# Kernel optimization log

Measured on AMD Instinct MI355X. Metric: run time of the kernel, lower is better.

The kernel has to match this reference:

```python
import jax, jax.numpy as jnp
import numpy as np

BS, S1, S2, D_IN1, D_IN2, ATTN_DIM, HEADS = 4, 2048, 2048, 512, 512, 512, 8
HEAD_DIM = ATTN_DIM // HEADS
NEG = -1e23


def _layer_norm(x, g, b, eps=1e-5):
    m = jnp.mean(x, axis=-1, keepdims=True)
    v = jnp.mean((x - m) ** 2, axis=-1, keepdims=True)
    return (x - m) / jnp.sqrt(v + eps) * g + b


def setup_inputs() -> dict:
    key = jax.random.key(0)
    ks = jax.random.split(key, 12)
    s = 0.02
    return {
        "modal1": jax.random.normal(ks[0], (BS, S1, D_IN1), dtype=jnp.float32),
        "modal2": jax.random.normal(ks[1], (BS, S2, D_IN2), dtype=jnp.float32),
        "unpadding_mask1": jax.random.randint(ks[2], (BS, S1, 1), 0, 2, dtype=jnp.int32),
        "unpadding_mask2": jax.random.randint(ks[3], (BS, S2), 0, 2, dtype=jnp.int32),
        "Wq": jax.random.normal(ks[4], (D_IN1, ATTN_DIM), dtype=jnp.float32) * s,
        "bq": jnp.zeros((ATTN_DIM,), dtype=jnp.float32),
        "Wkv": jax.random.normal(ks[5], (D_IN2, ATTN_DIM), dtype=jnp.float32) * s,
        "bkv": jnp.zeros((ATTN_DIM,), dtype=jnp.float32),
        "ln1_g": jnp.ones((ATTN_DIM,), dtype=jnp.float32),
        "ln1_b": jnp.zeros((ATTN_DIM,), dtype=jnp.float32),
        "W1": jax.random.normal(ks[6], (ATTN_DIM, ATTN_DIM), dtype=jnp.float32) * s,
        "b1": jnp.zeros((ATTN_DIM,), dtype=jnp.float32),
        "W2": jax.random.normal(ks[7], (ATTN_DIM, ATTN_DIM), dtype=jnp.float32) * s,
        "b2": jnp.zeros((ATTN_DIM,), dtype=jnp.float32),
        "ln2_g": jnp.ones((ATTN_DIM,), dtype=jnp.float32),
        "ln2_b": jnp.zeros((ATTN_DIM,), dtype=jnp.float32),
    }


def reference(modal1, modal2, unpadding_mask1, unpadding_mask2,
              Wq, bq, Wkv, bkv, ln1_g, ln1_b, W1, b1, W2, b2, ln2_g, ln2_b):
    bs = modal1.shape[0]
    q = modal1 @ Wq + bq                       # (bs, s1, D)
    kv = modal2 @ Wkv + bkv                    # (bs, s2, D)
    q = q.reshape(bs, -1, HEADS, HEAD_DIM).transpose(0, 2, 1, 3)    # (bs,h,s1,hd)
    k = kv.reshape(bs, -1, HEADS, HEAD_DIM).transpose(0, 2, 1, 3)   # (bs,h,s2,hd)
    v = k                                       # original reuses k as v (no v_proj)
    # padding mask: (bs,s1,1) x (bs,1,s2) -> (bs,s1,s2) > 0
    m1 = unpadding_mask1.astype(jnp.float32)            # (bs, s1, 1)
    m2 = unpadding_mask2.astype(jnp.float32)[:, None, :]  # (bs, 1, s2)
    attn_mask = (m1 @ m2) > 0                            # (bs, s1, s2)
    scale = 1.0 / (float(ATTN_DIM) ** 0.5)               # NOTE: attn_dim, not head_dim
    logits = jnp.einsum('bhqd,bhkd->bhqk', q, k) * scale
    logits = logits + jnp.where(attn_mask[:, None, :, :], 0.0, NEG)
    attn = jax.nn.softmax(logits, axis=-1)
    attn_res = jnp.einsum('bhqk,bhkd->bhqd', attn, v)
    attn_res = attn_res.transpose(0, 2, 1, 3).reshape(bs, -1, ATTN_DIM)
    # dropout in eval mode == identity
    x = attn_res + modal1
    x = _layer_norm(x, ln1_g, ln1_b)
    residual = x
    _ffn_out = jnp.tanh(x @ W1 + b1) @ W2 + b2  # computed then DISCARDED (original bug)
    x = attn_res + residual                      # x = dropout(attn_res) + residual
    x = _layer_norm(x, ln2_g, ln2_b)
    return x
```

## Files before the change

kernel.cpp:

```cpp
#include <hip/hip_runtime.h>
#include <hip/hip_bf16.h>

#define BSZ 4
#define S1v 2048
#define S2v 2048
#define DM 512
#define NH 8
#define HD 64
#define SCALE 0.044194173824159216f
#define L2E 1.4426950408889634f
#define SC_L2E (0.044194173824159216f * 1.4426950408889634f)
#define CBIAS 0.0028152f
#define NEGB (-1e30f)

typedef __bf16 bf16x8 __attribute__((ext_vector_type(8)));
typedef float f32x4 __attribute__((ext_vector_type(4)));

__device__ __forceinline__ unsigned short f2bf(float f) {
  union { float f; unsigned u; } v; v.f = f;
  unsigned r = v.u + 0x7FFFu + ((v.u >> 16) & 1u);
  return (unsigned short)(r >> 16);
}
__device__ __forceinline__ unsigned asu(float f) {
  union { float f; unsigned u; } v; v.f = f; return v.u;
}

__global__ __launch_bounds__(256)
void wtrans(const float* __restrict__ W, unsigned short* __restrict__ Wt) {
  __shared__ float tile[32][33];
  const int tx = threadIdx.x, ty = threadIdx.y;
  const int n0 = blockIdx.x * 32, k0 = blockIdx.y * 32;
#pragma unroll
  for (int i = 0; i < 32; i += 8)
    tile[ty + i][tx] = W[(size_t)(k0 + ty + i) * DM + n0 + tx];
  __syncthreads();
#pragma unroll
  for (int i = 0; i < 32; i += 8)
    Wt[(size_t)(n0 + ty + i) * DM + k0 + tx] = f2bf(tile[tx][ty + i]);
}

__global__ __launch_bounds__(256)
void proj_gemm(const float* __restrict__ X, const unsigned short* __restrict__ Wt,
               const float* __restrict__ bias, unsigned short* __restrict__ Y) {
  __shared__ unsigned short Xs[128][72];
  __shared__ unsigned short Ws[128][72];
  const int tid = threadIdx.x;
  const int wv = tid >> 6, lane = tid & 63;
  const int ln = lane & 15, qd = lane >> 4, q8 = qd * 8;
  const int wm = (wv >> 1) * 64, wn = (wv & 1) * 64;
  const int m0 = blockIdx.x * 128, n0 = blockIdx.y * 128;
  f32x4 acc[4][4] = {};
  for (int k0 = 0; k0 < DM; k0 += 64) {
    __syncthreads();
#pragma unroll
    for (int i = 0; i < 8; ++i) {
      int cid = tid + i * 256;
      int r = cid >> 4, c4 = (cid & 15) * 4;
      const float4 v = *(const float4*)(X + (size_t)(m0 + r) * DM + k0 + c4);
      ushort4 bv;
      bv.x = f2bf(v.x); bv.y = f2bf(v.y); bv.z = f2bf(v.z); bv.w = f2bf(v.w);
      *(ushort4*)&Xs[r][c4] = bv;
    }
#pragma unroll
    for (int i = 0; i < 4; ++i) {
      int cid = tid + i * 256;
      int r = cid >> 3, ch = (cid & 7) * 8;
      *(uint4*)&Ws[r][ch] = *(const uint4*)(Wt + (size_t)(n0 + r) * DM + k0 + ch);
    }
    __syncthreads();
#pragma unroll
    for (int kk = 0; kk < 2; ++kk) {
      bf16x8 aF[4], bF[4];
#pragma unroll
      for (int i = 0; i < 4; ++i)
        aF[i] = *(const bf16x8*)&Xs[wm + 16 * i + ln][kk * 32 + q8];
#pragma unroll
      for (int j = 0; j < 4; ++j)
        bF[j] = *(const bf16x8*)&Ws[wn + 16 * j + ln][kk * 32 + q8];
#pragma unroll
      for (int i = 0; i < 4; ++i)
#pragma unroll
        for (int j = 0; j < 4; ++j)
          acc[i][j] = __builtin_amdgcn_mfma_f32_16x16x32_bf16(aF[i], bF[j], acc[i][j], 0, 0, 0);
    }
  }
#pragma unroll
  for (int i = 0; i < 4; ++i)
#pragma unroll
    for (int j = 0; j < 4; ++j) {
      const int n = n0 + wn + 16 * j + ln;
      const float bb = bias[n];
#pragma unroll
      for (int r = 0; r < 4; ++r) {
        const int m = m0 + wm + 16 * i + qd * 4 + r;
        Y[(size_t)m * DM + n] = f2bf(acc[i][j][r] + bb);
      }
    }
}

__global__ __launch_bounds__(256)
void ktrans(const unsigned short* __restrict__ K, unsigned short* __restrict__ Kt) {
  __shared__ unsigned short T[128][72];
  const int tid = threadIdx.x;
  const int bh = blockIdx.y, b = bh >> 3, h = bh & 7;
  const int s0 = blockIdx.x * 128;
#pragma unroll
  for (int i = 0; i < 4; ++i) {
    int cid = tid + i * 256;
    int r = cid >> 3, ch = (cid & 7) * 8;
    *(uint4*)&T[r][ch] =
        *(const uint4*)(K + (size_t)(b * S2v + s0 + r) * DM + h * HD + ch);
  }
  __syncthreads();
#pragma unroll
  for (int i = 0; i < 4; ++i) {
    int cid = tid + i * 256;
    int d = cid >> 4, a = cid & 15;
    const int base = 16 * (a >> 2) + 4 * (a & 3);
    ushort4 v0, v1;
    v0.x = T[base + 0][d]; v0.y = T[base + 1][d];
    v0.z = T[base + 2][d]; v0.w = T[base + 3][d];
    v1.x = T[base + 64][d]; v1.y = T[base + 65][d];
    v1.z = T[base + 66][d]; v1.w = T[base + 67][d];
    unsigned short* o = Kt + ((size_t)(bh * HD + d)) * (size_t)S2v + s0 + a * 8;
    *(ushort4*)o = v0;
    *(ushort4*)(o + 4) = v1;
  }
}

__global__ __launch_bounds__(256, 3)
void flash_attn(const unsigned short* __restrict__ Qb, const unsigned short* __restrict__ Kb,
                const unsigned short* __restrict__ Kt, const int* __restrict__ m1,
                const int* __restrict__ m2, float* __restrict__ attn) {
  __shared__ unsigned short Ks[128][72];
  __shared__ unsigned short Vts[64][136];
  __shared__ float m2f[128];

  const int tid = threadIdx.x;
  const int wv = tid >> 6, lane = tid & 63;
  const int ln = lane & 15, qd = lane >> 4, q8 = qd * 8;
  const int lin = blockIdx.x + (blockIdx.y << 4);
  const int lid = ((lin & 7) << 6) | (lin >> 3);
  const int bh = lid >> 4;
  const int b = bh >> 3, h = bh & 7;
  const int q0 = (lid & 15) << 7;

  bf16x8 aQ[2][2];
#pragma unroll
  for (int t = 0; t < 2; ++t) {
    const size_t rbase =
        ((size_t)(b * S1v + q0 + wv * 32 + t * 16 + ln)) * DM + h * HD;
    aQ[t][0] = *(const bf16x8*)(Qb + rbase + q8);
    aQ[t][1] = *(const bf16x8*)(Qb + rbase + 32 + q8);
  }

  float acoef[2];
#pragma unroll
  for (int t = 0; t < 2; ++t)
    acoef[t] = (m1[b * S1v + q0 + wv * 32 + t * 16 + ln] == 0) ? 0.f : 1.f;

  float lrow[2] = {};
  f32x4 O[2][4] = {};

  for (int s0 = 0; s0 < S2v; s0 += 128) {
    __syncthreads();
#pragma unroll
    for (int i = 0; i < 4; ++i) {
      int cid = tid + i * 256;
      int r = cid >> 3, ch = (cid & 7) * 8;
      *(uint4*)&Ks[r][ch] =
          *(const uint4*)(Kb + ((size_t)(b * S2v + s0 + r)) * DM + h * HD + ch);
    }
#pragma unroll
    for (int i = 0; i < 4; ++i) {
      int cid = tid + i * 256;
      int r = cid >> 4, ch = (cid & 15) * 8;
      *(uint4*)&Vts[r][ch] =
          *(const uint4*)(Kt + ((size_t)(bh * HD + r)) * (size_t)S2v + s0 + ch);
    }
    if (tid < 128) m2f[tid] = (m2[b * S2v + s0 + tid] != 0) ? 0.f : NEGB;
    __syncthreads();

    f32x4 sc[2][8];
#pragma unroll
    for (int j = 0; j < 8; ++j) {
      const bf16x8 k0f = *(const bf16x8*)&Ks[16 * j + ln][q8];
      const bf16x8 k1f = *(const bf16x8*)&Ks[16 * j + ln][32 + q8];
#pragma unroll
      for (int t = 0; t < 2; ++t) {
        f32x4 z = {};
        z = __builtin_amdgcn_mfma_f32_16x16x32_bf16(k0f, aQ[t][0], z, 0, 0, 0);
        sc[t][j] = __builtin_amdgcn_mfma_f32_16x16x32_bf16(k1f, aQ[t][1], z, 0, 0, 0);
      }
    }

#pragma unroll
    for (int j = 0; j < 8; ++j) {
      const f32x4 mv = *(const f32x4*)&m2f[16 * j + 4 * qd];
#pragma unroll
      for (int t = 0; t < 2; ++t)
#pragma unroll
        for (int r = 0; r < 4; ++r) {
          const float e = fmaf(acoef[t], fmaf(sc[t][j][r], SC_L2E, mv[r]), CBIAS);
          const float p = __builtin_amdgcn_exp2f(e);
          lrow[t] += p;
          sc[t][j][r] = p;
        }
    }

#pragma unroll
    for (int kk = 0; kk < 4; ++kk) {
      bf16x8 aP[2];
#pragma unroll
      for (int t = 0; t < 2; ++t) {
        union { uint4 u; bf16x8 v; } cvt;
        cvt.u.x = __builtin_amdgcn_perm(asu(sc[t][kk][1]),     asu(sc[t][kk][0]),     0x07060302u);
        cvt.u.y = __builtin_amdgcn_perm(asu(sc[t][kk][3]),     asu(sc[t][kk][2]),     0x07060302u);
        cvt.u.z = __builtin_amdgcn_perm(asu(sc[t][kk + 4][1]), asu(sc[t][kk + 4][0]), 0x07060302u);
        cvt.u.w = __builtin_amdgcn_perm(asu(sc[t][kk + 4][3]), asu(sc[t][kk + 4][2]), 0x07060302u);
        aP[t] = cvt.v;
      }
#pragma unroll
      for (int jn = 0; jn < 4; ++jn) {
        const bf16x8 bV = *(const bf16x8*)&Vts[16 * jn + ln][kk * 32 + q8];
        O[0][jn] = __builtin_amdgcn_mfma_f32_16x16x32_bf16(aP[0], bV, O[0][jn], 0, 0, 0);
        O[1][jn] = __builtin_amdgcn_mfma_f32_16x16x32_bf16(aP[1], bV, O[1][jn], 0, 0, 0);
      }
    }
  }

  float inv[2];
#pragma unroll
  for (int t = 0; t < 2; ++t) {
    float l = lrow[t];
    l += __shfl_xor(l, 16, 64);
    l += __shfl_xor(l, 32, 64);
    inv[t] = l > 0.f ? 1.0f / l : 0.f;
  }
#pragma unroll
  for (int t = 0; t < 2; ++t)
#pragma unroll
    for (int r = 0; r < 4; ++r) {
      const float invr = __shfl(inv[t], 4 * qd + r, 64);
      const int m = q0 + wv * 32 + t * 16 + qd * 4 + r;
#pragma unroll
      for (int jn = 0; jn < 4; ++jn)
        attn[((size_t)(b * S1v + m)) * DM + h * HD + 16 * jn + ln] = O[t][jn][r] * invr;
    }
}

__global__ __launch_bounds__(128)
void ln_fused(const float* __restrict__ attn, const float* __restrict__ modal1,
              const float* __restrict__ g1, const float* __restrict__ b1,
              const float* __restrict__ g2, const float* __restrict__ b2,
              float* __restrict__ out) {
  __shared__ float red[4];
  const int row = blockIdx.x, t = threadIdx.x;
  const size_t base = (size_t)row * DM + t * 4;
  const float4 a = *(const float4*)(attn + base);
  const float4 mo = *(const float4*)(modal1 + base);
  float av[4] = { a.x, a.y, a.z, a.w };
  float x[4] = { a.x + mo.x, a.y + mo.y, a.z + mo.z, a.w + mo.w };
  float s = 0.f, q = 0.f;
#pragma unroll
  for (int i = 0; i < 4; ++i) { s += x[i]; q += x[i] * x[i]; }
#pragma unroll
  for (int m = 1; m < 64; m <<= 1) { s += __shfl_xor(s, m, 64); q += __shfl_xor(q, m, 64); }
  if ((t & 63) == 0) { red[t >> 6] = s; red[2 + (t >> 6)] = q; }
  __syncthreads();
  s = red[0] + red[1]; q = red[2] + red[3];
  const float mu = s * (1.0f / DM);
  const float rinv = rsqrtf(q * (1.0f / DM) - mu * mu + 1e-5f);
  const int c = t * 4;
  const float4 G1 = *(const float4*)(g1 + c), B1 = *(const float4*)(b1 + c);
  const float gg1[4] = { G1.x, G1.y, G1.z, G1.w }, bb1[4] = { B1.x, B1.y, B1.z, B1.w };
  float y[4];
  float s2 = 0.f, q2 = 0.f;
#pragma unroll
  for (int i = 0; i < 4; ++i) {
    y[i] = av[i] + (x[i] - mu) * rinv * gg1[i] + bb1[i];
    s2 += y[i]; q2 += y[i] * y[i];
  }
#pragma unroll
  for (int m = 1; m < 64; m <<= 1) { s2 += __shfl_xor(s2, m, 64); q2 += __shfl_xor(q2, m, 64); }
  __syncthreads();
  if ((t & 63) == 0) { red[t >> 6] = s2; red[2 + (t >> 6)] = q2; }
  __syncthreads();
  s2 = red[0] + red[1]; q2 = red[2] + red[3];
  const float mu2 = s2 * (1.0f / DM);
  const float rinv2 = rsqrtf(q2 * (1.0f / DM) - mu2 * mu2 + 1e-5f);
  const float4 G2 = *(const float4*)(g2 + c), B2 = *(const float4*)(b2 + c);
  float4 o;
  o.x = (y[0] - mu2) * rinv2 * G2.x + B2.x;
  o.y = (y[1] - mu2) * rinv2 * G2.y + B2.y;
  o.z = (y[2] - mu2) * rinv2 * G2.z + B2.z;
  o.w = (y[3] - mu2) * rinv2 * G2.w + B2.w;
  *(float4*)(out + base) = o;
}

extern "C" void kernel_launch(void* const* d_in, const int* in_sizes, int n_in,
                              void* d_out, int out_size, void* d_ws, size_t ws_size,
                              hipStream_t stream) {
  const float* modal1 = (const float*)d_in[0];
  const float* modal2 = (const float*)d_in[1];
  const int*   m1     = (const int*)d_in[2];
  const int*   m2     = (const int*)d_in[3];
  const float* Wq     = (const float*)d_in[4];
  const float* bq     = (const float*)d_in[5];
  const float* Wkv    = (const float*)d_in[6];
  const float* bkv    = (const float*)d_in[7];
  const float* g1     = (const float*)d_in[8];
  const float* b1     = (const float*)d_in[9];
  const float* g2     = (const float*)d_in[14];
  const float* b2     = (const float*)d_in[15];
  float* out = (float*)d_out;

  char* ws = (char*)d_ws;
  unsigned short* q_bf  = (unsigned short*)(ws);
  unsigned short* k_bf  = (unsigned short*)(ws + 8388608);
  unsigned short* kt_bf = (unsigned short*)(ws + 16777216);
  unsigned short* wqt   = (unsigned short*)(ws + 25165824);
  unsigned short* wkt   = (unsigned short*)(ws + 25690112);
  float*          attn  = (float*)(ws + 26214400);

  dim3 tb(32, 8);
  wtrans<<<dim3(16, 16), tb, 0, stream>>>(Wq, wqt);
  wtrans<<<dim3(16, 16), tb, 0, stream>>>(Wkv, wkt);
  proj_gemm<<<dim3(64, 4), 256, 0, stream>>>(modal1, wqt, bq, q_bf);
  proj_gemm<<<dim3(64, 4), 256, 0, stream>>>(modal2, wkt, bkv, k_bf);
  ktrans<<<dim3(16, 32), 256, 0, stream>>>(k_bf, kt_bf);
  flash_attn<<<dim3(16, 32), 256, 0, stream>>>(q_bf, k_bf, kt_bf, m1, m2, attn);
  ln_fused<<<dim3(8192), 128, 0, stream>>>(attn, modal1, g1, b1, g2, b2, out);
}
```

Measured before the change: 201.5 us.

## Double-buffer K/V tiles in flash attention and batch projection launches

The flash attention loop now double-buffers the K, V-transposed and mask tiles in shared memory. The next tile is loaded into registers before the current tile's MFMA work and written to the alternate buffer afterwards, so each iteration needs one barrier instead of two and global latency overlaps compute. The two weight-transpose launches and the two projection GEMM launches are each merged into a single launch using blockIdx.z, which cuts launch overhead and fills the GPU better for the small GEMMs. The costs are doubled LDS use, extra prefetch registers, and lowering the flash kernel's launch-bounds occupancy hint from 3 to 2 blocks.

After: 183.5 us. 1.1x faster.

```diff
diff --git a/kernel.cpp b/kernel.cpp
--- a/kernel.cpp
+++ b/kernel.cpp
@@ -26,8 +26,11 @@
 }
 
 __global__ __launch_bounds__(256)
-void wtrans(const float* __restrict__ W, unsigned short* __restrict__ Wt) {
+void wtrans(const float* __restrict__ W0, const float* __restrict__ W1,
+            unsigned short* __restrict__ T0, unsigned short* __restrict__ T1) {
   __shared__ float tile[32][33];
+  const float* W = blockIdx.z ? W1 : W0;
+  unsigned short* Wt = blockIdx.z ? T1 : T0;
   const int tx = threadIdx.x, ty = threadIdx.y;
   const int n0 = blockIdx.x * 32, k0 = blockIdx.y * 32;
 #pragma unroll
@@ -40,10 +43,16 @@
 }
 
 __global__ __launch_bounds__(256)
-void proj_gemm(const float* __restrict__ X, const unsigned short* __restrict__ Wt,
-               const float* __restrict__ bias, unsigned short* __restrict__ Y) {
+void proj_gemm(const float* __restrict__ X0, const float* __restrict__ X1,
+               const unsigned short* __restrict__ Wt0, const unsigned short* __restrict__ Wt1,
+               const float* __restrict__ bias0, const float* __restrict__ bias1,
+               unsigned short* __restrict__ Y0, unsigned short* __restrict__ Y1) {
   __shared__ unsigned short Xs[128][72];
   __shared__ unsigned short Ws[128][72];
+  const float* X = blockIdx.z ? X1 : X0;
+  const unsigned short* Wt = blockIdx.z ? Wt1 : Wt0;
+  const float* bias = blockIdx.z ? bias1 : bias0;
+  unsigned short* Y = blockIdx.z ? Y1 : Y0;
   const int tid = threadIdx.x;
   const int wv = tid >> 6, lane = tid & 63;
   const int ln = lane & 15, qd = lane >> 4, q8 = qd * 8;
@@ -128,13 +137,13 @@
   }
 }
 
-__global__ __launch_bounds__(256, 3)
+__global__ __launch_bounds__(256, 2)
 void flash_attn(const unsigned short* __restrict__ Qb, const unsigned short* __restrict__ Kb,
                 const unsigned short* __restrict__ Kt, const int* __restrict__ m1,
                 const int* __restrict__ m2, float* __restrict__ attn) {
-  __shared__ unsigned short Ks[128][72];
-  __shared__ unsigned short Vts[64][136];
-  __shared__ float m2f[128];
+  __shared__ unsigned short Ks[2][128][72];
+  __shared__ unsigned short Vts[2][64][136];
+  __shared__ float m2f[2][128];
 
   const int tid = threadIdx.x;
   const int wv = tid >> 6, lane = tid & 63;
@@ -145,6 +154,11 @@
   const int b = bh >> 3, h = bh & 7;
   const int q0 = (lid & 15) << 7;
 
+  const int rK = tid >> 3, cK = (tid & 7) * 8;
+  const int rV = tid >> 4, cV = (tid & 15) * 8;
+  const unsigned short* kbase = Kb + ((size_t)(b * S2v) + rK) * DM + h * HD + cK;
+  const unsigned short* vbase = Kt + ((size_t)(bh * HD + rV)) * (size_t)S2v + cV;
+
   bf16x8 aQ[2][2];
 #pragma unroll
   for (int t = 0; t < 2; ++t) {
@@ -162,30 +176,37 @@
   float lrow[2] = {};
   f32x4 O[2][4] = {};
 
-  for (int s0 = 0; s0 < S2v; s0 += 128) {
-    __syncthreads();
-#pragma unroll
-    for (int i = 0; i < 4; ++i) {
-      int cid = tid + i * 256;
-      int r = cid >> 3, ch = (cid & 7) * 8;
-      *(uint4*)&Ks[r][ch] =
-          *(const uint4*)(Kb + ((size_t)(b * S2v + s0 + r)) * DM + h * HD + ch);
-    }
-#pragma unroll
-    for (int i = 0; i < 4; ++i) {
-      int cid = tid + i * 256;
-      int r = cid >> 4, ch = (cid & 15) * 8;
-      *(uint4*)&Vts[r][ch] =
-          *(const uint4*)(Kt + ((size_t)(bh * HD + r)) * (size_t)S2v + s0 + ch);
-    }
-    if (tid < 128) m2f[tid] = (m2[b * S2v + s0 + tid] != 0) ? 0.f : NEGB;
-    __syncthreads();
+#pragma unroll
+  for (int i = 0; i < 4; ++i)
+    *(uint4*)&Ks[0][rK + i * 32][cK] = *(const uint4*)(kbase + (size_t)(i * 32) * DM);
+#pragma unroll
+  for (int i = 0; i < 4; ++i)
+    *(uint4*)&Vts[0][rV + i * 16][cV] =
+        *(const uint4*)(vbase + (size_t)(i * 16) * (size_t)S2v);
+  if (tid < 128) m2f[0][tid] = (m2[b * S2v + tid] != 0) ? 0.f : NEGB;
+  __syncthreads();
+
+  for (int it = 0; it < 16; ++it) {
+    const int cur = it & 1;
+    const bool pf = (it != 15);
+
+    uint4 nk[4], nv[4]; float nm = 0.f;
+    if (pf) {
+      const int sn = (it + 1) << 7;
+#pragma unroll
+      for (int i = 0; i < 4; ++i)
+        nk[i] = *(const uint4*)(kbase + ((size_t)sn + (size_t)(i * 32)) * DM);
+#pragma unroll
+      for (int i = 0; i < 4; ++i)
+        nv[i] = *(const uint4*)(vbase + sn + (size_t)(i * 16) * (size_t)S2v);
+      if (tid < 128) nm = (m2[b * S2v + sn + tid] != 0) ? 0.f : NEGB;
+    }
 
     f32x4 sc[2][8];
 #pragma unroll
     for (int j = 0; j < 8; ++j) {
-      const bf16x8 k0f = *(const bf16x8*)&Ks[16 * j + ln][q8];
-      const bf16x8 k1f = *(const bf16x8*)&Ks[16 * j + ln][32 + q8];
+      const bf16x8 k0f = *(const bf16x8*)&Ks[cur][16 * j + ln][q8];
+      const bf16x8 k1f = *(const bf16x8*)&Ks[cur][16 * j + ln][32 + q8];
 #pragma unroll
       for (int t = 0; t < 2; ++t) {
         f32x4 z = {};
@@ -196,7 +217,7 @@
 
 #pragma unroll
     for (int j = 0; j < 8; ++j) {
-      const f32x4 mv = *(const f32x4*)&m2f[16 * j + 4 * qd];
+      const f32x4 mv = *(const f32x4*)&m2f[cur][16 * j + 4 * qd];
 #pragma unroll
       for (int t = 0; t < 2; ++t)
 #pragma unroll
@@ -222,10 +243,19 @@
       }
 #pragma unroll
       for (int jn = 0; jn < 4; ++jn) {
-        const bf16x8 bV = *(const bf16x8*)&Vts[16 * jn + ln][kk * 32 + q8];
+        const bf16x8 bV = *(const bf16x8*)&Vts[cur][16 * jn + ln][kk * 32 + q8];
         O[0][jn] = __builtin_amdgcn_mfma_f32_16x16x32_bf16(aP[0], bV, O[0][jn], 0, 0, 0);
         O[1][jn] = __builtin_amdgcn_mfma_f32_16x16x32_bf16(aP[1], bV, O[1][jn], 0, 0, 0);
       }
+    }
+
+    if (pf) {
+#pragma unroll
+      for (int i = 0; i < 4; ++i) *(uint4*)&Ks[cur ^ 1][rK + i * 32][cK] = nk[i];
+#pragma unroll
+      for (int i = 0; i < 4; ++i) *(uint4*)&Vts[cur ^ 1][rV + i * 16][cV] = nv[i];
+      if (tid < 128) m2f[cur ^ 1][tid] = nm;
+      __syncthreads();
     }
   }
 
@@ -324,10 +354,9 @@
   float*          attn  = (float*)(ws + 26214400);
 
   dim3 tb(32, 8);
-  wtrans<<<dim3(16, 16), tb, 0, stream>>>(Wq, wqt);
-  wtrans<<<dim3(16, 16), tb, 0, stream>>>(Wkv, wkt);
-  proj_gemm<<<dim3(64, 4), 256, 0, stream>>>(modal1, wqt, bq, q_bf);
-  proj_gemm<<<dim3(64, 4), 256, 0, stream>>>(modal2, wkt, bkv, k_bf);
+  wtrans<<<dim3(16, 16, 2), tb, 0, stream>>>(Wq, Wkv, wqt, wkt);
+  proj_gemm<<<dim3(64, 4, 2), 256, 0, stream>>>(modal1, modal2, wqt, wkt,
+                                                bq, bkv, q_bf, k_bf);
   ktrans<<<dim3(16, 32), 256, 0, stream>>>(k_bf, kt_bf);
   flash_attn<<<dim3(16, 32), 256, 0, stream>>>(q_bf, k_bf, kt_bf, m1, m2, attn);
   ln_fused<<<dim3(8192), 128, 0, stream>>>(attn, modal1, g1, b1, g2, b2, out);
```
